# Optimization experiments

Measured on AMD Instinct MI355X. Metric: run time of the kernel, lower is better.

Reference implementation:

```python
import jax, jax.numpy as jnp
import numpy as np

B, F, H, N, S, L, E = 32, 128, 256, 2048, 3, 2, 262144
DEG = E // (B * N)  # average degree used to normalize position updates


def setup_inputs() -> dict:
    key = jax.random.key(0)
    ks = jax.random.split(key, 12)
    s = 0.05
    return {
        "x": jax.random.normal(ks[0], (B, F), jnp.float32),
        "positions": jax.random.normal(ks[1], (N, S), jnp.float32),
        "W_in": jax.random.normal(ks[2], (F, H), jnp.float32) * s,
        "b_in": jnp.zeros((H,), jnp.float32),
        "Wg1": jax.random.normal(ks[3], (3, H // 2), jnp.float32) * s,
        "bg1": jnp.zeros((H // 2,), jnp.float32),
        "Wg2": jax.random.normal(ks[4], (H // 2, H), jnp.float32) * s,
        "bg2": jnp.zeros((H,), jnp.float32),
        "Wm": jax.random.normal(ks[5], (L, 2 * H + 1, H), jnp.float32) * s,
        "bm": jnp.zeros((L, H), jnp.float32),
        "Wu": jax.random.normal(ks[6], (L, 2 * H, H), jnp.float32) * s,
        "bu": jnp.zeros((L, H), jnp.float32),
        "Wp": jax.random.normal(ks[7], (L, H, 1), jnp.float32) * s,
        "W_out": jax.random.normal(ks[8], (H, 1), jnp.float32) * s,
        "b_out": jnp.zeros((1,), jnp.float32),
        "edge_index": jax.random.randint(ks[9], (2, E), 0, B * N, dtype=jnp.int32),
    }


def _geometric_features(positions, Wg1, bg1, Wg2, bg2):
    # For single points, pairwise / centroid / Hausdorff distances all reduce to
    # the euclidean distance, so feature[i, 0..2] = mean_{j != i} ||p_i - p_j||.
    n = positions.shape[0]
    diff = positions[:, None, :] - positions[None, :, :]      # [N, N, S]
    dsq = jnp.sum(diff * diff, axis=-1)                        # [N, N]
    mask = 1.0 - jnp.eye(n, dtype=positions.dtype)
    d = jnp.sqrt(jnp.where(mask > 0, dsq, 1.0)) * mask         # grad-safe sqrt
    mean_d = jnp.sum(d, axis=1) / (n - 1)                      # [N]
    gf = jnp.stack([mean_d, mean_d, mean_d], axis=-1)          # [N, 3]
    return jax.nn.relu(gf @ Wg1 + bg1) @ Wg2 + bg2             # [N, H]


def _forward(x, positions, W_in, b_in, Wg1, bg1, Wg2, bg2, Wm, bm, Wu, bu, Wp, W_out, b_out, edge_index):
    nn_ = B * N
    h = x @ W_in + b_in                                        # [B, H]
    h = jnp.broadcast_to(h[:, None, :], (B, N, H)).reshape(nn_, H)
    pos = jnp.broadcast_to(positions[None], (B, N, S)).reshape(nn_, S)
    g = _geometric_features(positions, Wg1, bg1, Wg2, bg2)     # [N, H]
    h = h + jnp.broadcast_to(g[None], (B, N, H)).reshape(nn_, H)
    src, dst = edge_index[0], edge_index[1]
    for l in range(L):  # small fixed layer loop
        dvec = pos[src] - pos[dst]
        d = jnp.sqrt(jnp.sum(dvec * dvec, axis=-1, keepdims=True) + 1e-12)  # [E, 1]
        m = jax.nn.relu(jnp.concatenate([h[src], h[dst], d], axis=-1) @ Wm[l] + bm[l])
        agg = jax.ops.segment_sum(m, dst, num_segments=nn_)    # [B*N, H]
        coef = m @ Wp[l]                                       # [E, 1]
        pos = pos + jax.ops.segment_sum((pos[dst] - pos[src]) * coef, dst, num_segments=nn_) / DEG
        h = h + jax.nn.relu(jnp.concatenate([h, agg], axis=-1) @ Wu[l] + bu[l])
    out = (h.reshape(B, N, H) @ W_out + b_out).squeeze(-1)     # [B, N]
    return out


def reference(x, positions, W_in, b_in, Wg1, bg1, Wg2, bg2, Wm, bm, Wu, bu, Wp, W_out, b_out, edge_index):
    return _forward(x, positions, W_in, b_in, Wg1, bg1, Wg2, bg2, Wm, bm, Wu, bu, Wp, W_out, b_out, edge_index)
```

## Files before the change

### kernel.cpp

```cpp
#include <hip/hip_runtime.h>
#include <math.h>

#define B_ 32
#define F_ 128
#define H_ 256
#define N_ 2048
#define L_ 2
#define E_ 262144
#define NN_ 65536

typedef __attribute__((ext_vector_type(8))) short short8;
typedef __attribute__((ext_vector_type(4))) float f32x4;
typedef __attribute__((ext_vector_type(2))) float f32x2;

static __device__ __forceinline__ unsigned short f2bf(float f) {
  unsigned int u = __float_as_uint(f);
  u += 0x7FFF + ((u >> 16) & 1);
  return (unsigned short)(u >> 16);
}
static __device__ __forceinline__ float bf2f(unsigned short u) {
  return __uint_as_float(((unsigned int)u) << 16);
}
static __device__ __forceinline__ unsigned int pk_bf16(float lo, float hi) {
  unsigned int r;
  asm("v_cvt_pk_bf16_f32 %0, %1, %2" : "=v"(r) : "v"(lo), "v"(hi));
  return r;
}

typedef const __attribute__((address_space(1))) unsigned int* as1p;
typedef __attribute__((address_space(3))) unsigned int* as3p;
static __device__ __forceinline__ void gload16(const void* g, void* l) {
  __builtin_amdgcn_global_load_lds((as1p)g, (as3p)l, 16, 0, 0);
}

__global__ void mega1_kernel(const int* __restrict__ ei, int* __restrict__ deg,
                             const float* __restrict__ Wm, const float* __restrict__ Wu,
                             unsigned short* __restrict__ Wt1, unsigned short* __restrict__ Wut,
                             const float* __restrict__ x, const float* __restrict__ W_in,
                             const float* __restrict__ b_in, float* __restrict__ h0,
                             const float* __restrict__ positions,
                             const float* __restrict__ Wg1, const float* __restrict__ bg1,
                             const float* __restrict__ Wg2, const float* __restrict__ bg2,
                             float* __restrict__ g) {
  __shared__ float red[256];
  __shared__ float hid[128];
  const int blk = blockIdx.x;
  const int t = threadIdx.x;
  if (blk < 1024) {
    int e = blk * 256 + t;
    atomicAdd(&deg[ei[E_ + e]], 1);
  } else if (blk < 1280) {
    int idx = (blk - 1024) * 256 + t;
    int sel = idx >> 14;
    int rem = idx & 16383;
    if (sel < 2) {
      const float* W = Wm + (size_t)sel * 513 * H_;
      unsigned short* dst = Wt1 + (size_t)sel * 131072 + ((size_t)rem << 3);
      int gg = rem >> 13;
      int r2 = rem & 8191;
      int kc = r2 >> 11, w = (r2 >> 9) & 3, ks = (r2 >> 8) & 1, ni = (r2 >> 6) & 3, lane = r2 & 63;
      int r = lane & 15, q = lane >> 4;
      int n  = (w << 6) + (ni << 4) + r;
      int kb = (gg << 8) + (kc << 6) + (ks << 5) + (q << 3);
#pragma unroll
      for (int j = 0; j < 8; ++j)
        dst[j] = f2bf(W[(size_t)(kb + j) * H_ + n]);
    } else {
      const float* W = Wu + (size_t)(sel - 2) * 512 * H_;
      unsigned short* dst = Wut + (size_t)(sel - 2) * 131072 + ((size_t)rem << 3);
      int kc = rem >> 11, w = (rem >> 9) & 3, ks = (rem >> 8) & 1, ni = (rem >> 6) & 3, lane = rem & 63;
      int r = lane & 15, q = lane >> 4;
      int n  = (w << 6) + (ni << 4) + r;
      int kb = (kc << 6) + (ks << 5) + (q << 3);
#pragma unroll
      for (int j = 0; j < 8; ++j)
        dst[j] = f2bf(W[(size_t)(kb + j) * H_ + n]);
    }
  } else if (blk < 1312) {
    int b = blk - 1280;
    float acc = b_in[t];
#pragma unroll 8
    for (int k = 0; k < F_; ++k)
      acc += x[b * F_ + k] * W_in[k * H_ + t];
    h0[b * H_ + t] = acc;
  } else {
    int n = blk - 1312;
    float px = positions[n * 3 + 0], py = positions[n * 3 + 1], pz = positions[n * 3 + 2];
    float s = 0.f;
    for (int j = t; j < N_; j += 256) {
      float dx = px - positions[j * 3 + 0];
      float dy = py - positions[j * 3 + 1];
      float dz = pz - positions[j * 3 + 2];
      s += sqrtf(dx * dx + dy * dy + dz * dz);
    }
    red[t] = s;
    __syncthreads();
    for (int off = 128; off > 0; off >>= 1) {
      if (t < off) red[t] += red[t + off];
      __syncthreads();
    }
    float md = red[0] / (float)(N_ - 1);
    if (t < 128) {
      float w = Wg1[t] + Wg1[128 + t] + Wg1[256 + t];
      hid[t] = fmaxf(md * w + bg1[t], 0.f);
    }
    __syncthreads();
    float acc = bg2[t];
#pragma unroll 8
    for (int k = 0; k < 128; ++k)
      acc += hid[k] * Wg2[k * H_ + t];
    g[n * H_ + t] = acc;
  }
}


__global__ void scan1_kernel(const int* __restrict__ deg, int* __restrict__ bsum) {
  __shared__ int red[256];
  int t = threadIdx.x;
  red[t] = deg[blockIdx.x * 256 + t];
  __syncthreads();
  for (int off = 128; off > 0; off >>= 1) {
    if (t < off) red[t] += red[t + off];
    __syncthreads();
  }
  if (t == 0) bsum[blockIdx.x] = red[0];
}

__global__ void scan2_kernel(int* __restrict__ bsum) {
  __shared__ int s[256];
  int t = threadIdx.x;
  s[t] = bsum[t];
  __syncthreads();
  for (int off = 1; off < 256; off <<= 1) {
    int v = (t >= off) ? s[t - off] : 0;
    __syncthreads();
    s[t] += v;
    __syncthreads();
  }
  bsum[t] = (t == 0) ? 0 : s[t - 1];
}

__global__ void mega2_kernel(const int* __restrict__ deg, const int* __restrict__ bsum,
                             int* __restrict__ cur, int* __restrict__ rowptr,
                             const float* __restrict__ h0, const float* __restrict__ g,
                             const float* __restrict__ positions,
                             unsigned short* __restrict__ hbf,
                             unsigned short* __restrict__ hg,
                             float* __restrict__ pos4) {
  __shared__ int s[256];
  const int blk0 = blockIdx.x;
  const int t = threadIdx.x;
  if (blk0 < 256) {
    int i = blk0 * 256 + t;
    s[t] = deg[i];
    __syncthreads();
    for (int off = 1; off < 256; off <<= 1) {
      int v = (t >= off) ? s[t - off] : 0;
      __syncthreads();
      s[t] += v;
      __syncthreads();
    }
    int excl = (t == 0) ? 0 : s[t - 1];
    int v = bsum[blk0] + excl;
    cur[i] = v;
    rowptr[i] = v;
    return;
  }
  const int blk = blk0 - 256;
  if (blk < 8192) {
    int idx = blk * 256 + t;
    int row = idx >> 5;
    int c8 = (idx & 31) << 3;
    const float* hp = h0 + (row >> 11) * H_ + c8;
    const float* gp = g + (row & (N_ - 1)) * H_ + c8;
    const float4 a = *(const float4*)hp;
    const float4 a2 = *(const float4*)(hp + 4);
    const float4 b = *(const float4*)gp;
    const float4 b2 = *(const float4*)(gp + 4);
    short8 v;
    v[0] = (short)f2bf(a.x + b.x);  v[1] = (short)f2bf(a.y + b.y);
    v[2] = (short)f2bf(a.z + b.z);  v[3] = (short)f2bf(a.w + b.w);
    v[4] = (short)f2bf(a2.x + b2.x); v[5] = (short)f2bf(a2.y + b2.y);
    v[6] = (short)f2bf(a2.z + b2.z); v[7] = (short)f2bf(a2.w + b2.w);
    *(short8*)(hbf + (((size_t)row) << 8) + c8) = v;
  } else if (blk < 8452) {
    int idx = (blk - 8192) * 256 + t;
    int row = idx >> 5;
    int c8 = (idx & 31) << 3;
    const float* src = (row < 2048) ? (g + (size_t)row * H_ + c8)
                                    : (h0 + (size_t)(row - 2048) * H_ + c8);
    const float4 a = *(const float4*)src;
    const float4 a2 = *(const float4*)(src + 4);
    short8 v;
    v[0] = (short)f2bf(a.x);  v[1] = (short)f2bf(a.y);
    v[2] = (short)f2bf(a.z);  v[3] = (short)f2bf(a.w);
    v[4] = (short)f2bf(a2.x); v[5] = (short)f2bf(a2.y);
    v[6] = (short)f2bf(a2.z); v[7] = (short)f2bf(a2.w);
    *(short8*)(hg + (((size_t)row) << 8) + c8) = v;
  } else {
    int n = (blk - 8452) * 256 + t;
    int src = (n & (N_ - 1)) * 3;
    float4 v;
    v.x = positions[src + 0];
    v.y = positions[src + 1];
    v.z = positions[src + 2];
    v.w = 0.f;
    *(float4*)(pos4 + ((size_t)n << 2)) = v;
  }
}


#define GEMM_IDS(BID)                                                \
  const int t = threadIdx.x;                                         \
  const int m0 = (BID) << 6;                                         \
  const int wu = __builtin_amdgcn_readfirstlane(t >> 6);             \
  const int lane = t & 63;                                           \
  const int q = lane >> 4;                                           \
  const int r = lane & 15;                                           \
  const int arow = lane >> 2;                                        \
  const int aq = (lane & 3) ^ ((lane >> 2) & 3);

#define STAGE_P(P, abase)                                                                \
  do {                                                                                   \
    gload16((abase) + (((size_t)(m0 + (wu << 4) + arow)) << 8) + (((P) & 7) << 5) +      \
                (aq << 3),                                                               \
            &sA[(P) & 3][wu << 9]);                                                      \
    _Pragma("unroll")                                                                    \
    for (int j_ = 0; j_ < 4; ++j_)                                                       \
      gload16(Wt + (((size_t)((P) >> 1)) << 14) + (wu << 12) + (((P) & 1) << 11) +       \
                  (j_ << 9) + (lane << 3),                                               \
              &sB[(P) & 3][(wu << 11) + (j_ << 9)]);                                     \
  } while (0)

#define COMPUTE_P(P)                                                                     \
  do {                                                                                   \
    short8 af[4], bfr[4];                                                                \
    _Pragma("unroll")                                                                    \
    for (int mi = 0; mi < 4; ++mi)                                                       \
      af[mi] = *(const short8*)(&sA[(P) & 3][((mi * 16 + r) << 5) +                      \
                                             ((q ^ (r & 3)) << 3)]);                     \
    _Pragma("unroll")                                                                    \
    for (int ni = 0; ni < 4; ++ni)                                                       \
      bfr[ni] = *(const short8*)(&sB[(P) & 3][(wu << 11) + (ni << 9) + (lane << 3)]);    \
    _Pragma("unroll")                                                                    \
    for (int mi = 0; mi < 4; ++mi)                                                       \
      _Pragma("unroll")                                                                  \
      for (int ni = 0; ni < 4; ++ni)                                                     \
        acc[mi][ni] = __builtin_amdgcn_mfma_f32_16x16x32_bf16(af[mi], bfr[ni],           \
                                                              acc[mi][ni], 0, 0, 0);     \
  } while (0)

#define WAIT_BAR(P)                                                       \
  do {                                                                    \
    if ((P) <= 13)      asm volatile("s_waitcnt vmcnt(10)" ::: "memory"); \
    else if ((P) == 14) asm volatile("s_waitcnt vmcnt(5)" ::: "memory");  \
    else                asm volatile("s_waitcnt vmcnt(0)" ::: "memory");  \
    __builtin_amdgcn_s_barrier();                                         \
    asm volatile("" ::: "memory");                                        \
  } while (0)

#define ACC_ZERO()                                   \
  _Pragma("unroll")                                  \
  for (int mi = 0; mi < 4; ++mi)                     \
    _Pragma("unroll")                                \
    for (int ni = 0; ni < 4; ++ni)                   \
      acc[mi][ni] = (f32x4){0.f, 0.f, 0.f, 0.f};

__launch_bounds__(256)
__global__ void mega3_kernel(const int* __restrict__ ei, int* __restrict__ cur,
                             int* __restrict__ src_s,
                             const unsigned short* __restrict__ hg,
                             const unsigned short* __restrict__ Wt,
                             const float* __restrict__ bm,
                             float* __restrict__ Xc, float* __restrict__ Zc) {
  __shared__ __align__(16) unsigned short sA[4][2048];
  __shared__ __align__(16) unsigned short sB[4][8192];
  const int blk = blockIdx.x;
  if (blk < 1024) {
    int e = blk * 256 + threadIdx.x;
    int s = ei[e], d = ei[E_ + e];
    int p = atomicAdd(&cur[d], 1);
    src_s[p] = s;
    return;
  }
  const int bid = blk - 1024;
  GEMM_IDS(bid)

  f32x4 acc[4][4];
  ACC_ZERO();

  STAGE_P(0, hg); STAGE_P(1, hg); STAGE_P(2, hg);
#pragma unroll
  for (int p = 0; p < 16; ++p) {
    WAIT_BAR(p);
    if (p + 3 < 16) STAGE_P(p + 3, hg);
    COMPUTE_P(p);
    if (p == 7) {
#pragma unroll
      for (int ni = 0; ni < 4; ++ni) {
        int n = (wu << 6) + ni * 16 + r;
#pragma unroll
        for (int mi = 0; mi < 4; ++mi)
#pragma unroll
          for (int reg = 0; reg < 4; ++reg) {
            size_t idx = (((size_t)(m0 + mi * 16 + q * 4 + reg)) << 8) + n;
            Xc[idx] = acc[mi][ni][reg];
            acc[mi][ni][reg] = 0.f;
          }
      }
    }
  }

  const int isH0 = (bid == 32);
#pragma unroll
  for (int ni = 0; ni < 4; ++ni) {
    int n = (wu << 6) + ni * 16 + r;
    float bmn = isH0 ? bm[n] : 0.f;
#pragma unroll
    for (int mi = 0; mi < 4; ++mi)
#pragma unroll
      for (int reg = 0; reg < 4; ++reg) {
        size_t idx = (((size_t)(m0 + mi * 16 + q * 4 + reg)) << 8) + n;
        Zc[idx] = acc[mi][ni][reg] + bmn;
      }
  }
}

__launch_bounds__(256)
__global__ void gemm1_mfma(const unsigned short* __restrict__ hbf,
                           const unsigned short* __restrict__ Wt,
                           const float* __restrict__ bm,
                           unsigned short* __restrict__ X, unsigned short* __restrict__ Zb) {
  __shared__ __align__(16) unsigned short sA[4][2048];
  __shared__ __align__(16) unsigned short sB[4][8192];
  GEMM_IDS(blockIdx.x)

  f32x4 acc[4][4];
  ACC_ZERO();

  STAGE_P(0, hbf); STAGE_P(1, hbf); STAGE_P(2, hbf);
#pragma unroll
  for (int p = 0; p < 16; ++p) {
    WAIT_BAR(p);
    if (p + 3 < 16) STAGE_P(p + 3, hbf);
    COMPUTE_P(p);
    if (p == 7) {
#pragma unroll
      for (int ni = 0; ni < 4; ++ni) {
        int n = (wu << 6) + ni * 16 + r;
#pragma unroll
        for (int mi = 0; mi < 4; ++mi)
#pragma unroll
          for (int reg = 0; reg < 4; ++reg) {
            size_t idx = (((size_t)(m0 + mi * 16 + q * 4 + reg)) << 8) + n;
            X[idx] = f2bf(acc[mi][ni][reg]);
            acc[mi][ni][reg] = 0.f;
          }
      }
    }
  }

#pragma unroll
  for (int ni = 0; ni < 4; ++ni) {
    int n = (wu << 6) + ni * 16 + r;
    float bmn = bm[n];
#pragma unroll
    for (int mi = 0; mi < 4; ++mi)
#pragma unroll
      for (int reg = 0; reg < 4; ++reg) {
        size_t idx = (((size_t)(m0 + mi * 16 + q * 4 + reg)) << 8) + n;
        Zb[idx] = f2bf(acc[mi][ni][reg] + bmn);
      }
  }
}

static __device__ __forceinline__ void edge_core(
    const float4 pn, const float4 q,
    f32x2 x01, f32x2 x23,
    const f32x2 z01, const f32x2 z23,
    const f32x2 wl01, const f32x2 wl23,
    const f32x2 wp01, const f32x2 wp23,
    f32x2& a01, f32x2& a23,
    float& pdx, float& pdy, float& pdz) {
  const float dx = pn.x - q.x, dy = pn.y - q.y, dz = pn.z - q.z;
  const float d = sqrtf(dx * dx + dy * dy + dz * dz + 1e-12f);
  f32x2 dd; dd[0] = d; dd[1] = d;
  f32x2 v01 = x01 + z01 + dd * wl01;
  f32x2 v23 = x23 + z23 + dd * wl23;
  v01[0] = fmaxf(v01[0], 0.f); v01[1] = fmaxf(v01[1], 0.f);
  v23[0] = fmaxf(v23[0], 0.f); v23[1] = fmaxf(v23[1], 0.f);
  a01 += v01; a23 += v23;
  const f32x2 cpv = v01 * wp01 + v23 * wp23;
  const float cp = cpv[0] + cpv[1];
  pdx += dx * cp; pdy += dy * cp; pdz += dz * cp;
}

static __device__ __forceinline__ void edge_do(
    const float4 pn, const float4 q, const uint2 xv,
    const f32x2 z01, const f32x2 z23,
    const f32x2 wl01, const f32x2 wl23,
    const f32x2 wp01, const f32x2 wp23,
    f32x2& a01, f32x2& a23,
    float& pdx, float& pdy, float& pdz) {
  f32x2 x01, x23;
  x01[0] = __uint_as_float(xv.x << 16);
  x01[1] = __uint_as_float(xv.x & 0xffff0000u);
  x23[0] = __uint_as_float(xv.y << 16);
  x23[1] = __uint_as_float(xv.y & 0xffff0000u);
  edge_core(pn, q, x01, x23, z01, z23, wl01, wl23, wp01, wp23, a01, a23, pdx, pdy, pdz);
}

static __device__ __forceinline__ void edge_do0(
    const float4 pn, const float4 q, const float4 xg, const float4 xh,
    const f32x2 z01, const f32x2 z23,
    const f32x2 wl01, const f32x2 wl23,
    const f32x2 wp01, const f32x2 wp23,
    f32x2& a01, f32x2& a23,
    float& pdx, float& pdy, float& pdz) {
  f32x2 x01, x23;
  x01[0] = xg.x + xh.x; x01[1] = xg.y + xh.y;
  x23[0] = xg.z + xh.z; x23[1] = xg.w + xh.w;
  edge_core(pn, q, x01, x23, z01, z23, wl01, wl23, wp01, wp23, a01, a23, pdx, pdy, pdz);
}

__launch_bounds__(256)
__global__ void edge_kernel(const unsigned short* __restrict__ X,
                            const unsigned short* __restrict__ Zb,
                            const float* __restrict__ pos_c,
                            const int* __restrict__ rowptr, const int* __restrict__ src_s,
                            const float* __restrict__ wl, const float* __restrict__ wp,
                            unsigned short* __restrict__ aggb, float* __restrict__ pos_o) {
  const int gid = blockIdx.x * 256 + threadIdx.x;
  const int n = __builtin_amdgcn_readfirstlane(gid >> 6);
  const int lane = threadIdx.x & 63;

  const float4 wlv = *(const float4*)(wl + (lane << 2));
  const float4 wpv = *(const float4*)(wp + (lane << 2));
  const f32x2 wl01 = {wlv.x, wlv.y}, wl23 = {wlv.z, wlv.w};
  const f32x2 wp01 = {wpv.x, wpv.y}, wp23 = {wpv.z, wpv.w};

  const int e0 = rowptr[n];
  const int e1 = (n == NN_ - 1) ? E_ : rowptr[n + 1];

  const uint2 zv = *(const uint2*)(Zb + (((size_t)n) << 8) + (lane << 2));
  f32x2 z01, z23;
  z01[0] = __uint_as_float(zv.x << 16);
  z01[1] = __uint_as_float(zv.x & 0xffff0000u);
  z23[0] = __uint_as_float(zv.y << 16);
  z23[1] = __uint_as_float(zv.y & 0xffff0000u);

  const float4 pn = *(const float4*)(pos_c + ((size_t)n << 2));
  f32x2 a01 = {0.f, 0.f}, a23 = {0.f, 0.f};
  float pdx = 0.f, pdy = 0.f, pdz = 0.f;

  const unsigned short* Xl = X + (lane << 2);

  int e = e0;
  for (; e + 4 <= e1; e += 4) {
    const int s0 = src_s[e], s1 = src_s[e + 1], s2 = src_s[e + 2], s3 = src_s[e + 3];
    const float4 q0 = *(const float4*)(pos_c + ((size_t)s0 << 2));
    const float4 q1 = *(const float4*)(pos_c + ((size_t)s1 << 2));
    const float4 q2 = *(const float4*)(pos_c + ((size_t)s2 << 2));
    const float4 q3 = *(const float4*)(pos_c + ((size_t)s3 << 2));
    const uint2 x0 = *(const uint2*)(Xl + (((size_t)s0) << 8));
    const uint2 x1 = *(const uint2*)(Xl + (((size_t)s1) << 8));
    const uint2 x2 = *(const uint2*)(Xl + (((size_t)s2) << 8));
    const uint2 x3 = *(const uint2*)(Xl + (((size_t)s3) << 8));
    edge_do(pn, q0, x0, z01, z23, wl01, wl23, wp01, wp23, a01, a23, pdx, pdy, pdz);
    edge_do(pn, q1, x1, z01, z23, wl01, wl23, wp01, wp23, a01, a23, pdx, pdy, pdz);
    edge_do(pn, q2, x2, z01, z23, wl01, wl23, wp01, wp23, a01, a23, pdx, pdy, pdz);
    edge_do(pn, q3, x3, z01, z23, wl01, wl23, wp01, wp23, a01, a23, pdx, pdy, pdz);
  }
  if (e + 2 <= e1) {
    const int s0 = src_s[e], s1 = src_s[e + 1];
    const float4 q0 = *(const float4*)(pos_c + ((size_t)s0 << 2));
    const float4 q1 = *(const float4*)(pos_c + ((size_t)s1 << 2));
    const uint2 x0 = *(const uint2*)(Xl + (((size_t)s0) << 8));
    const uint2 x1 = *(const uint2*)(Xl + (((size_t)s1) << 8));
    edge_do(pn, q0, x0, z01, z23, wl01, wl23, wp01, wp23, a01, a23, pdx, pdy, pdz);
    edge_do(pn, q1, x1, z01, z23, wl01, wl23, wp01, wp23, a01, a23, pdx, pdy, pdz);
    e += 2;
  }
  if (e < e1) {
    const int s0 = src_s[e];
    const float4 q0 = *(const float4*)(pos_c + ((size_t)s0 << 2));
    const uint2 x0 = *(const uint2*)(Xl + (((size_t)s0) << 8));
    edge_do(pn, q0, x0, z01, z23, wl01, wl23, wp01, wp23, a01, a23, pdx, pdy, pdz);
  }

  uint2 av;
  av.x = pk_bf16(a01[0], a01[1]);
  av.y = pk_bf16(a23[0], a23[1]);
  *(uint2*)(aggb + (((size_t)n) << 8) + (lane << 2)) = av;

#pragma unroll
  for (int m = 1; m < 64; m <<= 1) {
    pdx += __shfl_xor(pdx, m, 64);
    pdy += __shfl_xor(pdy, m, 64);
    pdz += __shfl_xor(pdz, m, 64);
  }
  if (lane == 0) {
    float4 po;
    po.x = pn.x + pdx * 0.25f;
    po.y = pn.y + pdy * 0.25f;
    po.z = pn.z + pdz * 0.25f;
    po.w = 0.f;
    *(float4*)(pos_o + ((size_t)n << 2)) = po;
  }
}

__launch_bounds__(256)
__global__ void edge0_kernel(const float* __restrict__ Xc,
                             const float* __restrict__ Zc,
                             const float* __restrict__ pos_c,
                             const int* __restrict__ rowptr, const int* __restrict__ src_s,
                             const float* __restrict__ wl, const float* __restrict__ wp,
                             unsigned short* __restrict__ aggb, float* __restrict__ pos_o) {
  const int gid = blockIdx.x * 256 + threadIdx.x;
  const int n = __builtin_amdgcn_readfirstlane(gid >> 6);
  const int lane = threadIdx.x & 63;

  const float4 wlv = *(const float4*)(wl + (lane << 2));
  const float4 wpv = *(const float4*)(wp + (lane << 2));
  const f32x2 wl01 = {wlv.x, wlv.y}, wl23 = {wlv.z, wlv.w};
  const f32x2 wp01 = {wpv.x, wpv.y}, wp23 = {wpv.z, wpv.w};

  const int e0 = rowptr[n];
  const int e1 = (n == NN_ - 1) ? E_ : rowptr[n + 1];

  const float* Xl = Xc + (lane << 2);
  const float* Zl = Zc + (lane << 2);

  const float4 zg = *(const float4*)(Zl + (((size_t)(n & (N_ - 1))) << 8));
  const float4 zh = *(const float4*)(Zl + (((size_t)(2048 + (n >> 11))) << 8));
  f32x2 z01, z23;
  z01[0] = zg.x + zh.x; z01[1] = zg.y + zh.y;
  z23[0] = zg.z + zh.z; z23[1] = zg.w + zh.w;

  const float4 pn = *(const float4*)(pos_c + ((size_t)n << 2));
  f32x2 a01 = {0.f, 0.f}, a23 = {0.f, 0.f};
  float pdx = 0.f, pdy = 0.f, pdz = 0.f;

  int e = e0;
  for (; e + 4 <= e1; e += 4) {
    const int s0 = src_s[e], s1 = src_s[e + 1], s2 = src_s[e + 2], s3 = src_s[e + 3];
    const float4 q0 = *(const float4*)(pos_c + ((size_t)s0 << 2));
    const float4 q1 = *(const float4*)(pos_c + ((size_t)s1 << 2));
    const float4 q2 = *(const float4*)(pos_c + ((size_t)s2 << 2));
    const float4 q3 = *(const float4*)(pos_c + ((size_t)s3 << 2));
    const float4 xg0 = *(const float4*)(Xl + (((size_t)(s0 & (N_ - 1))) << 8));
    const float4 xh0 = *(const float4*)(Xl + (((size_t)(2048 + (s0 >> 11))) << 8));
    const float4 xg1 = *(const float4*)(Xl + (((size_t)(s1 & (N_ - 1))) << 8));
    const float4 xh1 = *(const float4*)(Xl + (((size_t)(2048 + (s1 >> 11))) << 8));
    const float4 xg2 = *(const float4*)(Xl + (((size_t)(s2 & (N_ - 1))) << 8));
    const float4 xh2 = *(const float4*)(Xl + (((size_t)(2048 + (s2 >> 11))) << 8));
    const float4 xg3 = *(const float4*)(Xl + (((size_t)(s3 & (N_ - 1))) << 8));
    const float4 xh3 = *(const float4*)(Xl + (((size_t)(2048 + (s3 >> 11))) << 8));
    edge_do0(pn, q0, xg0, xh0, z01, z23, wl01, wl23, wp01, wp23, a01, a23, pdx, pdy, pdz);
    edge_do0(pn, q1, xg1, xh1, z01, z23, wl01, wl23, wp01, wp23, a01, a23, pdx, pdy, pdz);
    edge_do0(pn, q2, xg2, xh2, z01, z23, wl01, wl23, wp01, wp23, a01, a23, pdx, pdy, pdz);
    edge_do0(pn, q3, xg3, xh3, z01, z23, wl01, wl23, wp01, wp23, a01, a23, pdx, pdy, pdz);
  }
  for (; e < e1; ++e) {
    const int s0 = src_s[e];
    const float4 q0 = *(const float4*)(pos_c + ((size_t)s0 << 2));
    const float4 xg0 = *(const float4*)(Xl + (((size_t)(s0 & (N_ - 1))) << 8));
    const float4 xh0 = *(const float4*)(Xl + (((size_t)(2048 + (s0 >> 11))) << 8));
    edge_do0(pn, q0, xg0, xh0, z01, z23, wl01, wl23, wp01, wp23, a01, a23, pdx, pdy, pdz);
  }

  uint2 av;
  av.x = pk_bf16(a01[0], a01[1]);
  av.y = pk_bf16(a23[0], a23[1]);
  *(uint2*)(aggb + (((size_t)n) << 8) + (lane << 2)) = av;

#pragma unroll
  for (int m = 1; m < 64; m <<= 1) {
    pdx += __shfl_xor(pdx, m, 64);
    pdy += __shfl_xor(pdy, m, 64);
    pdz += __shfl_xor(pdz, m, 64);
  }
  if (lane == 0) {
    float4 po;
    po.x = pn.x + pdx * 0.25f;
    po.y = pn.y + pdy * 0.25f;
    po.z = pn.z + pdz * 0.25f;
    po.w = 0.f;
    *(float4*)(pos_o + ((size_t)n << 2)) = po;
  }
}

__launch_bounds__(256)
__global__ void upd2_mfma(unsigned short* __restrict__ hbf,
                          const unsigned short* __restrict__ aggb,
                          const unsigned short* __restrict__ Wt,
                          const float* __restrict__ bu) {
  __shared__ __align__(16) unsigned short sA[4][2048];
  __shared__ __align__(16) unsigned short sB[4][8192];
  GEMM_IDS(blockIdx.x)

  f32x4 acc[4][4];
  ACC_ZERO();

  const unsigned short* hb = (const unsigned short*)hbf;
  STAGE_P(0, hb); STAGE_P(1, hb); STAGE_P(2, hb);
#pragma unroll
  for (int p = 0; p < 16; ++p) {
    WAIT_BAR(p);
    if (p + 3 < 16) {
      const unsigned short* ab = (p + 3 < 8) ? hb : aggb;
      STAGE_P(p + 3, ab);
    }
    COMPUTE_P(p);
  }

#pragma unroll
  for (int ni = 0; ni < 4; ++ni) {
    int n = (wu << 6) + ni * 16 + r;
    float buv = bu[n];
#pragma unroll
    for (int mi = 0; mi < 4; ++mi)
#pragma unroll
      for (int reg = 0; reg < 4; ++reg) {
        size_t idx = (((size_t)(m0 + mi * 16 + q * 4 + reg)) << 8) + n;
        float v = bf2f(hbf[idx]) + fmaxf(acc[mi][ni][reg] + buv, 0.f);
        hbf[idx] = f2bf(v);
      }
  }
}

__launch_bounds__(256)
__global__ void upd2_out(const unsigned short* __restrict__ hbf,
                         const unsigned short* __restrict__ aggb,
                         const unsigned short* __restrict__ Wt,
                         const float* __restrict__ bu,
                         const float* __restrict__ Wout, const float* __restrict__ bout,
                         float* __restrict__ out) {
  __shared__ __align__(16) unsigned short sA[4][2048];
  __shared__ __align__(16) unsigned short sB[4][8192];
  GEMM_IDS(blockIdx.x)

  f32x4 acc[4][4];
  ACC_ZERO();

  STAGE_P(0, hbf); STAGE_P(1, hbf); STAGE_P(2, hbf);
#pragma unroll
  for (int p = 0; p < 16; ++p) {
    WAIT_BAR(p);
    if (p + 3 < 16) {
      const unsigned short* ab = (p + 3 < 8) ? hbf : aggb;
      STAGE_P(p + 3, ab);
    }
    COMPUTE_P(p);
  }
  __syncthreads();
  float (*sRed)[64] = (float(*)[64])(&sA[0][0]);

  float dotp[4][4];
#pragma unroll
  for (int mi = 0; mi < 4; ++mi)
#pragma unroll
    for (int reg = 0; reg < 4; ++reg)
      dotp[mi][reg] = 0.f;

#pragma unroll
  for (int ni = 0; ni < 4; ++ni) {
    int n = (wu << 6) + ni * 16 + r;
    float buv = bu[n];
    float won = Wout[n];
#pragma unroll
    for (int mi = 0; mi < 4; ++mi)
#pragma unroll
      for (int reg = 0; reg < 4; ++reg) {
        size_t idx = (((size_t)(m0 + mi * 16 + q * 4 + reg)) << 8) + n;
        float v = bf2f(hbf[idx]) + fmaxf(acc[mi][ni][reg] + buv, 0.f);
        dotp[mi][reg] += v * won;
      }
  }
#pragma unroll
  for (int mask = 1; mask < 16; mask <<= 1)
#pragma unroll
    for (int mi = 0; mi < 4; ++mi)
#pragma unroll
      for (int reg = 0; reg < 4; ++reg)
        dotp[mi][reg] += __shfl_xor(dotp[mi][reg], mask, 64);
  if (r == 0) {
#pragma unroll
    for (int mi = 0; mi < 4; ++mi)
#pragma unroll
      for (int reg = 0; reg < 4; ++reg)
        sRed[wu][mi * 16 + q * 4 + reg] = dotp[mi][reg];
  }
  __syncthreads();
  if (t < 64)
    out[m0 + t] = sRed[0][t] + sRed[1][t] + sRed[2][t] + sRed[3][t] + bout[0];
}


extern "C" void kernel_launch(void* const* d_in, const int* in_sizes, int n_in,
                              void* d_out, int out_size, void* d_ws, size_t ws_size,
                              hipStream_t stream) {
  const float* x         = (const float*)d_in[0];
  const float* positions = (const float*)d_in[1];
  const float* W_in      = (const float*)d_in[2];
  const float* b_in      = (const float*)d_in[3];
  const float* Wg1       = (const float*)d_in[4];
  const float* bg1       = (const float*)d_in[5];
  const float* Wg2       = (const float*)d_in[6];
  const float* bg2       = (const float*)d_in[7];
  const float* Wm        = (const float*)d_in[8];
  const float* bm        = (const float*)d_in[9];
  const float* Wu        = (const float*)d_in[10];
  const float* bu        = (const float*)d_in[11];
  const float* Wp        = (const float*)d_in[12];
  const float* W_out     = (const float*)d_in[13];
  const float* b_out     = (const float*)d_in[14];
  const int*   ei        = (const int*)d_in[15];
  float* out = (float*)d_out;

  char* ws = (char*)d_ws;
  unsigned short* hbf   = (unsigned short*)(ws);
  unsigned short* X     = (unsigned short*)(ws +  33554432UL);
  unsigned short* Zb    = (unsigned short*)(ws +  67108864UL);
  unsigned short* aggb  = (unsigned short*)(ws + 100663296UL);
  float*          posA  = (float*)(ws + 134217728UL);
  float*          posB  = (float*)(ws + 135266304UL);
  float*          g     = (float*)(ws + 136314880UL);
  float*          h0    = (float*)(ws + 138412032UL);
  unsigned short* Wt1   = (unsigned short*)(ws + 138444800UL);
  unsigned short* Wut   = (unsigned short*)(ws + 138969088UL);
  int*            deg   = (int*)(ws + 139493376UL);
  int*            cur   = (int*)(ws + 139755520UL);
  int*            bsum  = (int*)(ws + 140017664UL);
  int*            rowptr= (int*)(ws + 140018688UL);
  int*            src_s = (int*)(ws + 140280832UL);

  unsigned short* hg = aggb;
  float*          Xc = (float*)X;
  float*          Zc = (float*)Zb;

  hipMemsetAsync(deg, 0, (size_t)NN_ * sizeof(int), stream);

  mega1_kernel<<<3360, 256, 0, stream>>>(ei, deg, Wm, Wu, Wt1, Wut,
                                         x, W_in, b_in, h0,
                                         positions, Wg1, bg1, Wg2, bg2, g);

  scan1_kernel<<<256, 256, 0, stream>>>(deg, bsum);
  scan2_kernel<<<1, 256, 0, stream>>>(bsum);

  mega2_kernel<<<8964, 256, 0, stream>>>(deg, bsum, cur, rowptr,
                                         h0, g, positions, hbf, hg, posA);

  mega3_kernel<<<1057, 256, 0, stream>>>(ei, cur, src_s, hg, Wt1, bm, Xc, Zc);

  edge0_kernel<<<NN_ / 4, 256, 0, stream>>>(Xc, Zc, posA, rowptr, src_s,
                                            Wm + 512 * H_, Wp, aggb, posB);
  upd2_mfma<<<NN_ / 64, 256, 0, stream>>>(hbf, aggb, Wut, bu);

  gemm1_mfma<<<NN_ / 64, 256, 0, stream>>>(hbf, Wt1 + 131072,
                                           bm + H_, X, Zb);
  edge_kernel<<<NN_ / 4, 256, 0, stream>>>(X, Zb, posB, rowptr, src_s,
                                           Wm + (size_t)513 * H_ + 512 * H_,
                                           Wp + H_, aggb, posA);
  upd2_out<<<NN_ / 64, 256, 0, stream>>>(hbf, aggb, Wut + 131072,
                                         bu + H_, W_out, b_out, out);
}
```

Measured before the change: 308.0 us.

## Decompose layer-0 update GEMM using low-rank structure of initial hidden state

Layer 0's hidden state is h0[b] + g[n], so the h-half of the update GEMM is split into a per-node term and a per-batch term. Both are precomputed once on the small hg matrix by extra blocks in mega3_kernel. upd2_dec then seeds its accumulators from those partials and runs only the K=256 aggregate half, halving the MFMA K-loop for the 1024-block update. The cost is extra fp32 Uc reads per element and 33 more blocks in mega3, and it relies on the hg row layout holding g rows followed by h0 rows.

```diff
diff --git a/kernel.cpp b/kernel.cpp
--- a/kernel.cpp
+++ b/kernel.cpp
@@ -259,6 +259,15 @@
     asm volatile("" ::: "memory");                                        \
   } while (0)
 
+#define WAIT_BAR8(P)                                                      \
+  do {                                                                    \
+    if ((P) <= 5)       asm volatile("s_waitcnt vmcnt(10)" ::: "memory"); \
+    else if ((P) == 6)  asm volatile("s_waitcnt vmcnt(5)" ::: "memory");  \
+    else                asm volatile("s_waitcnt vmcnt(0)" ::: "memory");  \
+    __builtin_amdgcn_s_barrier();                                         \
+    asm volatile("" ::: "memory");                                        \
+  } while (0)
+
 #define ACC_ZERO()                                   \
   _Pragma("unroll")                                  \
   for (int mi = 0; mi < 4; ++mi)                     \
@@ -270,9 +279,11 @@
 __global__ void mega3_kernel(const int* __restrict__ ei, int* __restrict__ cur,
                              int* __restrict__ src_s,
                              const unsigned short* __restrict__ hg,
-                             const unsigned short* __restrict__ Wt,
+                             const unsigned short* __restrict__ Wtm,
+                             const unsigned short* __restrict__ Wtu,
                              const float* __restrict__ bm,
-                             float* __restrict__ Xc, float* __restrict__ Zc) {
+                             float* __restrict__ Xc, float* __restrict__ Zc,
+                             float* __restrict__ Uc) {
   __shared__ __align__(16) unsigned short sA[4][2048];
   __shared__ __align__(16) unsigned short sB[4][8192];
   const int blk = blockIdx.x;
@@ -283,46 +294,77 @@
     src_s[p] = s;
     return;
   }
-  const int bid = blk - 1024;
-  GEMM_IDS(bid)
-
-  f32x4 acc[4][4];
-  ACC_ZERO();
-
-  STAGE_P(0, hg); STAGE_P(1, hg); STAGE_P(2, hg);
-#pragma unroll
-  for (int p = 0; p < 16; ++p) {
-    WAIT_BAR(p);
-    if (p + 3 < 16) STAGE_P(p + 3, hg);
-    COMPUTE_P(p);
-    if (p == 7) {
-#pragma unroll
-      for (int ni = 0; ni < 4; ++ni) {
-        int n = (wu << 6) + ni * 16 + r;
-#pragma unroll
-        for (int mi = 0; mi < 4; ++mi)
-#pragma unroll
-          for (int reg = 0; reg < 4; ++reg) {
-            size_t idx = (((size_t)(m0 + mi * 16 + q * 4 + reg)) << 8) + n;
-            Xc[idx] = acc[mi][ni][reg];
-            acc[mi][ni][reg] = 0.f;
-          }
+  if (blk < 1057) {
+    const int bid = blk - 1024;
+    const unsigned short* Wt = Wtm;
+    GEMM_IDS(bid)
+
+    f32x4 acc[4][4];
+    ACC_ZERO();
+
+    STAGE_P(0, hg); STAGE_P(1, hg); STAGE_P(2, hg);
+#pragma unroll
+    for (int p = 0; p < 16; ++p) {
+      WAIT_BAR(p);
+      if (p + 3 < 16) STAGE_P(p + 3, hg);
+      COMPUTE_P(p);
+      if (p == 7) {
+#pragma unroll
+        for (int ni = 0; ni < 4; ++ni) {
+          int n = (wu << 6) + ni * 16 + r;
+#pragma unroll
+          for (int mi = 0; mi < 4; ++mi)
+#pragma unroll
+            for (int reg = 0; reg < 4; ++reg) {
+              size_t idx = (((size_t)(m0 + mi * 16 + q * 4 + reg)) << 8) + n;
+              Xc[idx] = acc[mi][ni][reg];
+              acc[mi][ni][reg] = 0.f;
+            }
+        }
       }
     }
-  }
-
-  const int isH0 = (bid == 32);
-#pragma unroll
-  for (int ni = 0; ni < 4; ++ni) {
-    int n = (wu << 6) + ni * 16 + r;
-    float bmn = isH0 ? bm[n] : 0.f;
-#pragma unroll
-    for (int mi = 0; mi < 4; ++mi)
-#pragma unroll
-      for (int reg = 0; reg < 4; ++reg) {
-        size_t idx = (((size_t)(m0 + mi * 16 + q * 4 + reg)) << 8) + n;
-        Zc[idx] = acc[mi][ni][reg] + bmn;
-      }
+
+    const int isH0 = (bid == 32);
+#pragma unroll
+    for (int ni = 0; ni < 4; ++ni) {
+      int n = (wu << 6) + ni * 16 + r;
+      float bmn = isH0 ? bm[n] : 0.f;
+#pragma unroll
+      for (int mi = 0; mi < 4; ++mi)
+#pragma unroll
+        for (int reg = 0; reg < 4; ++reg) {
+          size_t idx = (((size_t)(m0 + mi * 16 + q * 4 + reg)) << 8) + n;
+          Zc[idx] = acc[mi][ni][reg] + bmn;
+        }
+    }
+    return;
+  }
+  {
+    const int bid = blk - 1057;
+    const unsigned short* Wt = Wtu;
+    GEMM_IDS(bid)
+
+    f32x4 acc[4][4];
+    ACC_ZERO();
+
+    STAGE_P(0, hg); STAGE_P(1, hg); STAGE_P(2, hg);
+#pragma unroll
+    for (int p = 0; p < 8; ++p) {
+      WAIT_BAR8(p);
+      if (p + 3 < 8) STAGE_P(p + 3, hg);
+      COMPUTE_P(p);
+    }
+#pragma unroll
+    for (int ni = 0; ni < 4; ++ni) {
+      int n = (wu << 6) + ni * 16 + r;
+#pragma unroll
+      for (int mi = 0; mi < 4; ++mi)
+#pragma unroll
+        for (int reg = 0; reg < 4; ++reg) {
+          size_t idx = (((size_t)(m0 + mi * 16 + q * 4 + reg)) << 8) + n;
+          Uc[idx] = acc[mi][ni][reg];
+        }
+    }
   }
 }
 
@@ -591,26 +633,37 @@
 }
 
 __launch_bounds__(256)
-__global__ void upd2_mfma(unsigned short* __restrict__ hbf,
-                          const unsigned short* __restrict__ aggb,
-                          const unsigned short* __restrict__ Wt,
-                          const float* __restrict__ bu) {
+__global__ void upd2_dec(unsigned short* __restrict__ hbf,
+                         const unsigned short* __restrict__ aggb,
+                         const unsigned short* __restrict__ Wt,
+                         const float* __restrict__ Uc,
+                         const float* __restrict__ bu) {
   __shared__ __align__(16) unsigned short sA[4][2048];
   __shared__ __align__(16) unsigned short sB[4][8192];
   GEMM_IDS(blockIdx.x)
 
+  const int nn0 = m0 & (N_ - 1);
+  const int bb  = m0 >> 11;
+
   f32x4 acc[4][4];
-  ACC_ZERO();
-
-  const unsigned short* hb = (const unsigned short*)hbf;
-  STAGE_P(0, hb); STAGE_P(1, hb); STAGE_P(2, hb);
-#pragma unroll
-  for (int p = 0; p < 16; ++p) {
-    WAIT_BAR(p);
-    if (p + 3 < 16) {
-      const unsigned short* ab = (p + 3 < 8) ? hb : aggb;
-      STAGE_P(p + 3, ab);
-    }
+#pragma unroll
+  for (int ni = 0; ni < 4; ++ni) {
+    int n = (wu << 6) + ni * 16 + r;
+    float uh = Uc[(((size_t)(2048 + bb)) << 8) + n];
+#pragma unroll
+    for (int mi = 0; mi < 4; ++mi)
+#pragma unroll
+      for (int reg = 0; reg < 4; ++reg) {
+        int rl = mi * 16 + q * 4 + reg;
+        acc[mi][ni][reg] = Uc[(((size_t)(nn0 + rl)) << 8) + n] + uh;
+      }
+  }
+
+  STAGE_P(0, aggb); STAGE_P(1, aggb); STAGE_P(2, aggb);
+#pragma unroll
+  for (int p = 0; p < 8; ++p) {
+    WAIT_BAR8(p);
+    if (p + 3 < 8) STAGE_P(p + 3, aggb);
     COMPUTE_P(p);
   }
 
@@ -734,6 +787,7 @@
   int*            bsum  = (int*)(ws + 140017664UL);
   int*            rowptr= (int*)(ws + 140018688UL);
   int*            src_s = (int*)(ws + 140280832UL);
+  float*          Uc    = (float*)(ws + 141329408UL);
 
   unsigned short* hg = aggb;
   float*          Xc = (float*)X;
@@ -751,11 +805,11 @@
   mega2_kernel<<<8964, 256, 0, stream>>>(deg, bsum, cur, rowptr,
                                          h0, g, positions, hbf, hg, posA);
 
-  mega3_kernel<<<1057, 256, 0, stream>>>(ei, cur, src_s, hg, Wt1, bm, Xc, Zc);
+  mega3_kernel<<<1090, 256, 0, stream>>>(ei, cur, src_s, hg, Wt1, Wut, bm, Xc, Zc, Uc);
 
   edge0_kernel<<<NN_ / 4, 256, 0, stream>>>(Xc, Zc, posA, rowptr, src_s,
                                             Wm + 512 * H_, Wp, aggb, posB);
-  upd2_mfma<<<NN_ / 64, 256, 0, stream>>>(hbf, aggb, Wut, bu);
+  upd2_dec<<<NN_ / 64, 256, 0, stream>>>(hbf, aggb, Wut + 65536, Uc, bu);
 
   gemm1_mfma<<<NN_ / 64, 256, 0, stream>>>(hbf, Wt1 + 131072,
                                            bm + H_, X, Zb);
```

Result: no change. 303.9 us (-1.3%).
